# Kernel optimization log

Hardware: AMD Instinct MI355X
Metric: run time of the kernel (lower is better)

Reference implementation:

```python
import jax, jax.numpy as jnp
import numpy as np

# Model config (matches init_kwargs)
B, S = 4, 1024          # batch of equal-length prefill sequences (cu_seqlens = arange(B+1)*S)
H, KVH, D = 16, 4, 64   # query heads, kv heads (GQA), head_dim
SCALE = 0.125           # 1/sqrt(head_dim)
NUM_SLOTS = 8192        # paged-KV-cache total slots


def setup_inputs() -> dict:
    key = jax.random.key(0)
    k1, k2, k3 = jax.random.split(key, 3)
    N = B * S
    q = jax.random.normal(k1, (N, H * D), dtype=jnp.float32)
    k = jax.random.normal(k2, (N, KVH * D), dtype=jnp.float32)
    v = jax.random.normal(k3, (N, KVH * D), dtype=jnp.float32)
    k_cache = jnp.zeros((NUM_SLOTS, KVH * D), dtype=jnp.float32)
    v_cache = jnp.zeros((NUM_SLOTS, KVH * D), dtype=jnp.float32)
    slot_mapping = jnp.arange(N, dtype=jnp.int32)  # valid slots, no -1 entries
    return {"q": q, "k": k, "v": v, "k_cache": k_cache, "v_cache": v_cache,
            "slot_mapping": slot_mapping}


def _varlen_causal_attn(q, k, v):
    # q: [N, H*D], k/v: [N, KVH*D]; equal-length varlen batch -> [B, S, ...]
    qh = q.reshape(B, S, H, D)
    kh = k.reshape(B, S, KVH, D)
    vh = v.reshape(B, S, KVH, D)
    rep = H // KVH  # GQA: repeat kv heads to match query heads
    kh = jnp.repeat(kh, rep, axis=2)
    vh = jnp.repeat(vh, rep, axis=2)
    scores = jnp.einsum('bqhd,bkhd->bhqk', qh, kh) * SCALE
    causal = jnp.tril(jnp.ones((S, S), dtype=bool))
    scores = jnp.where(causal, scores, jnp.finfo(scores.dtype).min)
    p = jax.nn.softmax(scores, axis=-1)
    o = jnp.einsum('bhqk,bkhd->bqhd', p, vh)
    return o.reshape(B * S, H * D)


def reference(q, k, v, k_cache, v_cache, slot_mapping):
    # store_kvcache: scatter new k/v rows into the paged caches (Triton kernel equivalent)
    k_cache = k_cache.at[slot_mapping].set(k)
    v_cache = v_cache.at[slot_mapping].set(v)
    # prefill path: flash_attn_varlen_func(q, k, v, causal=True) on the fresh k/v
    o = _varlen_causal_attn(q, k, v)
    return o, k_cache, v_cache
```

## Files before the change

kernel.cpp:

```cpp
#include <hip/hip_runtime.h>
#include <hip/hip_bf16.h>

#define B_     4
#define S_     1024
#define H_     16
#define KVH_   4
#define D_     64
#define N_     (B_*S_)
#define SLOTS_ 8192
#define KVD_   (KVH_*D_)
#define HD_    (H_*D_)
#define SCL    (0.125f * 1.44269504f)

typedef __attribute__((ext_vector_type(8))) short bf16x8;
typedef __attribute__((ext_vector_type(4))) short bf16x4;
typedef __attribute__((ext_vector_type(4))) float f32x4;

__device__ __forceinline__ short4 f4tob4(float4 f){
    union { __hip_bfloat162 h[2]; short4 s; } u;
    u.h[0] = __float22bfloat162_rn(make_float2(f.x, f.y));
    u.h[1] = __float22bfloat162_rn(make_float2(f.z, f.w));
    return u.s;
}
__device__ __forceinline__ int swz(int row, int col){
    return row*64 + (col ^ ((row & 7) << 3));
}

__global__ __launch_bounds__(256) void copy_caches(
    const float4* __restrict__ kcin, const float4* __restrict__ vcin,
    float4* __restrict__ kc, float4* __restrict__ vc){
    int i = blockIdx.x*256 + threadIdx.x;
    kc[i] = kcin[i];
    vc[i] = vcin[i];
}

__global__ __launch_bounds__(256) void prep_kernel(
    const float* __restrict__ k, const float* __restrict__ v,
    const int* __restrict__ slot_map,
    float* __restrict__ kc, float* __restrict__ vc,
    short* __restrict__ Kb, short* __restrict__ Vtb)
{
    __shared__ short sv[64*68];
    const int tid = threadIdx.x;
    const int g   = blockIdx.x >> 4;
    const int s0  = (blockIdx.x & 15) * 64;
    const int b   = g >> 2, kvh = g & 3;

    const int sl = tid >> 2;
    const int cq = (tid & 3) * 16;

    const int n   = b*S_ + s0 + sl;
    const int pos = s0 + sl;
    const float4* kp = (const float4*)(k + (size_t)n*KVD_ + kvh*D_ + cq);
    const float4* vp = (const float4*)(v + (size_t)n*KVD_ + kvh*D_ + cq);
    const int s = slot_map[n];

    float4 kk[4], vv[4];
    #pragma unroll
    for (int j = 0; j < 4; ++j){ kk[j] = kp[j]; vv[j] = vp[j]; }

    if (s >= 0){
        float4* kcp = (float4*)(kc + (size_t)s*KVD_ + kvh*D_ + cq);
        float4* vcp = (float4*)(vc + (size_t)s*KVD_ + kvh*D_ + cq);
        #pragma unroll
        for (int j = 0; j < 4; ++j){ kcp[j] = kk[j]; vcp[j] = vv[j]; }
    }

    short* kbp = Kb + ((size_t)g*S_ + pos)*64 + cq;
    #pragma unroll
    for (int j = 0; j < 4; ++j)
        *(short4*)(kbp + j*4) = f4tob4(kk[j]);

    #pragma unroll
    for (int j = 0; j < 4; ++j)
        *(short4*)(&sv[sl*68 + cq + j*4]) = f4tob4(vv[j]);
    __syncthreads();

    const int d  = tid >> 2;
    const int sg = (tid & 3) * 16;
    union { short s[16]; bf16x8 v8[2]; } out;
    #pragma unroll
    for (int i = 0; i < 16; ++i)
        out.s[i] = sv[(sg + i)*68 + d];
    short* vtp = Vtb + ((size_t)g*64 + d)*S_ + s0 + sg;
    *(bf16x8*)(vtp)     = out.v8[0];
    *(bf16x8*)(vtp + 8) = out.v8[1];
}

__global__ __launch_bounds__(256, 2) void attn_kernel(
    const float* __restrict__ q, const short* __restrict__ Kb,
    const short* __restrict__ Vtb, float* __restrict__ o)
{
    __shared__ __align__(16) short sK[2][64*64];
    __shared__ __align__(16) short sV[2][64*64];

    const int tid  = threadIdx.x;
    const int wave = tid >> 6;
    const int lane = tid & 63;
    const int quad = lane >> 4;
    const int l16  = lane & 15;

    const int bid = blockIdx.x;
    const int g   = bid & 15;
    const int p   = bid >> 4;
    const int qtA = p, qtB = 63 - p;
    const int ntA = (qtA >> 2) + 1;
    const int ntB = (qtB >> 2) + 1;

    const int b = g >> 2, kvh = g & 3;
    const int h = kvh*4 + wave;

    bf16x8 qfA[2], qfB[2];
    {
        const float* qpA = q + ((size_t)(b*S_ + qtA*16 + l16))*HD_ + h*D_ + quad*8;
        const float* qpB = q + ((size_t)(b*S_ + qtB*16 + l16))*HD_ + h*D_ + quad*8;
        #pragma unroll
        for (int ks = 0; ks < 2; ++ks){
            float4 a0 = *(const float4*)(qpA + ks*32);
            float4 a1 = *(const float4*)(qpA + ks*32 + 4);
            float4 b0 = *(const float4*)(qpB + ks*32);
            float4 b1 = *(const float4*)(qpB + ks*32 + 4);
            a0.x*=SCL; a0.y*=SCL; a0.z*=SCL; a0.w*=SCL;
            a1.x*=SCL; a1.y*=SCL; a1.z*=SCL; a1.w*=SCL;
            b0.x*=SCL; b0.y*=SCL; b0.z*=SCL; b0.w*=SCL;
            b1.x*=SCL; b1.y*=SCL; b1.z*=SCL; b1.w*=SCL;
            union { short4 s[2]; bf16x8 v8; } ua, ub;
            ua.s[0] = f4tob4(a0); ua.s[1] = f4tob4(a1);
            ub.s[0] = f4tob4(b0); ub.s[1] = f4tob4(b1);
            qfA[ks] = ua.v8; qfB[ks] = ub.v8;
        }
    }

    f32x4 ofA[4], ofB[4];
    #pragma unroll
    for (int f2 = 0; f2 < 4; ++f2){
        ofA[f2] = (f32x4){0.f,0.f,0.f,0.f};
        ofB[f2] = (f32x4){0.f,0.f,0.f,0.f};
    }
    float lsA = 0.f, lsB = 0.f;
    const int qrowA = qtA*16 + l16, qrowB = qtB*16 + l16;

    const short* Kg = Kb  + (size_t)g*S_*64;
    const short* Vg = Vtb + (size_t)g*64*S_;

    const int rs = tid >> 2;
    const int cg = (tid & 3) * 16;

    bf16x8 kst[2], vst[2];
    kst[0] = *(const bf16x8*)(Kg + (size_t)rs*64 + cg);
    kst[1] = *(const bf16x8*)(Kg + (size_t)rs*64 + cg + 8);
    vst[0] = *(const bf16x8*)(Vg + (size_t)rs*S_ + cg);
    vst[1] = *(const bf16x8*)(Vg + (size_t)rs*S_ + cg + 8);

    auto pv_body = [&](const f32x4* sc, f32x4* of, float& lsum,
                       int qrow, bool diag, int t, const short* V_){
        bf16x4 pfrag[4];
        #pragma unroll
        for (int f = 0; f < 4; ++f){
            float4 pf;
            #pragma unroll
            for (int r = 0; r < 4; ++r){
                float pe = __builtin_amdgcn_exp2f(sc[f][r]);
                if (diag && (t*64 + f*16 + quad*4 + r > qrow)) pe = 0.f;
                lsum += pe;
                ((float*)&pf)[r] = pe;
            }
            union { short4 s; bf16x4 bv; } u; u.s = f4tob4(pf);
            pfrag[f] = u.bv;
        }
        #pragma unroll
        for (int f = 0; f < 4; ++f){
            #pragma unroll
            for (int f2 = 0; f2 < 4; ++f2){
                bf16x4 vf = *(const bf16x4*)(&V_[swz(f2*16 + l16, f*16 + quad*4)]);
                of[f2] = __builtin_amdgcn_mfma_f32_16x16x16bf16_1k(pfrag[f], vf, of[f2], 0, 0, 0);
            }
        }
    };

    for (int t = 0; t < ntB; ++t){
        short* K_ = (short*)sK[t & 1];
        short* V_ = (short*)sV[t & 1];
        *(bf16x8*)(&K_[swz(rs, cg)])     = kst[0];
        *(bf16x8*)(&K_[swz(rs, cg + 8)]) = kst[1];
        *(bf16x8*)(&V_[swz(rs, cg)])     = vst[0];
        *(bf16x8*)(&V_[swz(rs, cg + 8)]) = vst[1];
        if (t + 1 < ntB){
            kst[0] = *(const bf16x8*)(Kg + (size_t)((t+1)*64 + rs)*64 + cg);
            kst[1] = *(const bf16x8*)(Kg + (size_t)((t+1)*64 + rs)*64 + cg + 8);
            vst[0] = *(const bf16x8*)(Vg + (size_t)rs*S_ + (t+1)*64 + cg);
            vst[1] = *(const bf16x8*)(Vg + (size_t)rs*S_ + (t+1)*64 + cg + 8);
        }
        __syncthreads();

        bf16x8 kf[2][4];
        #pragma unroll
        for (int ks = 0; ks < 2; ++ks)
            #pragma unroll
            for (int f = 0; f < 4; ++f)
                kf[ks][f] = *(const bf16x8*)(&K_[swz(f*16 + l16, ks*32 + quad*8)]);

        const bool actA = (t < ntA);

        f32x4 scB[4];
        #pragma unroll
        for (int f = 0; f < 4; ++f) scB[f] = (f32x4){0.f,0.f,0.f,0.f};
        #pragma unroll
        for (int ks = 0; ks < 2; ++ks)
            #pragma unroll
            for (int f = 0; f < 4; ++f)
                scB[f] = __builtin_amdgcn_mfma_f32_16x16x32_bf16(kf[ks][f], qfB[ks], scB[f], 0, 0, 0);
        pv_body(scB, ofB, lsB, qrowB, t == ntB - 1, t, V_);

        if (actA){
            f32x4 scA[4];
            #pragma unroll
            for (int f = 0; f < 4; ++f) scA[f] = (f32x4){0.f,0.f,0.f,0.f};
            #pragma unroll
            for (int ks = 0; ks < 2; ++ks)
                #pragma unroll
                for (int f = 0; f < 4; ++f)
                    scA[f] = __builtin_amdgcn_mfma_f32_16x16x32_bf16(kf[ks][f], qfA[ks], scA[f], 0, 0, 0);
            pv_body(scA, ofA, lsA, qrowA, t == ntA - 1, t, V_);
        }
    }

    auto epilogue = [&](f32x4* of, float lsum, int qt){
        lsum += __shfl_xor(lsum, 16);
        lsum += __shfl_xor(lsum, 32);
        float linv[4];
        #pragma unroll
        for (int r = 0; r < 4; ++r)
            linv[r] = 1.f / __shfl(lsum, quad*4 + r);
        #pragma unroll
        for (int f2 = 0; f2 < 4; ++f2){
            #pragma unroll
            for (int r = 0; r < 4; ++r){
                const int row = qt*16 + quad*4 + r;
                o[((size_t)(b*S_ + row))*HD_ + h*D_ + f2*16 + l16] = of[f2][r] * linv[r];
            }
        }
    };
    epilogue(ofA, lsA, qtA);
    epilogue(ofB, lsB, qtB);
}

extern "C" void kernel_launch(void* const* d_in, const int* in_sizes, int n_in,
                              void* d_out, int out_size, void* d_ws, size_t ws_size,
                              hipStream_t stream){
    (void)in_sizes; (void)n_in; (void)out_size; (void)ws_size;
    const float* q     = (const float*)d_in[0];
    const float* k     = (const float*)d_in[1];
    const float* v     = (const float*)d_in[2];
    const float* kc_in = (const float*)d_in[3];
    const float* vc_in = (const float*)d_in[4];
    const int*   slot  = (const int*)d_in[5];

    float* o  = (float*)d_out;
    float* kc = o + (size_t)N_*HD_;
    float* vc = kc + (size_t)SLOTS_*KVD_;

    short* Kb = (short*)d_ws;
    short* Vt = Kb + (size_t)16*S_*64;

    copy_caches<<<(SLOTS_*64)/256, 256, 0, stream>>>(
        (const float4*)kc_in, (const float4*)vc_in, (float4*)kc, (float4*)vc);

    prep_kernel<<<256, 256, 0, stream>>>(k, v, slot, kc, vc, Kb, Vt);

    attn_kernel<<<512, 256, 0, stream>>>(q, Kb, Vt, o);
}
```

Measured before the change: 116.7 us.

## Fuse cache scatter into attention launch via inverse slot map, split heads per block

Replaces the standalone cache copy and the scatter inside prep with an inverse slot map, built by extra prep blocks. Extra blocks appended to the attention launch then write each cache row once, from either the new k/v or the old cache. This removes the copy-then-overwrite double write and lets the cache traffic overlap attention compute. Attention blocks shrink to 128 threads covering two heads, doubling the block count. The QK and PV phases for the two query tiles are interleaved to share V fragment loads. It adds an init kernel, and the split means K/V tiles are loaded into LDS twice per group.

```diff
diff --git a/kernel.cpp b/kernel.cpp
--- a/kernel.cpp
+++ b/kernel.cpp
@@ -12,6 +12,9 @@
 #define HD_    (H_*D_)
 #define SCL    (0.125f * 1.44269504f)
 
+#define NATT   1024
+#define NCACHE 4096
+
 typedef __attribute__((ext_vector_type(8))) short bf16x8;
 typedef __attribute__((ext_vector_type(4))) short bf16x4;
 typedef __attribute__((ext_vector_type(4))) float f32x4;
@@ -26,22 +29,23 @@
     return row*64 + (col ^ ((row & 7) << 3));
 }
 
-__global__ __launch_bounds__(256) void copy_caches(
-    const float4* __restrict__ kcin, const float4* __restrict__ vcin,
-    float4* __restrict__ kc, float4* __restrict__ vc){
-    int i = blockIdx.x*256 + threadIdx.x;
-    kc[i] = kcin[i];
-    vc[i] = vcin[i];
+__global__ void inv_init(int* __restrict__ inv){
+    inv[blockIdx.x*256 + threadIdx.x] = -1;
 }
 
 __global__ __launch_bounds__(256) void prep_kernel(
     const float* __restrict__ k, const float* __restrict__ v,
-    const int* __restrict__ slot_map,
-    float* __restrict__ kc, float* __restrict__ vc,
+    const int* __restrict__ slot_map, int* __restrict__ inv,
     short* __restrict__ Kb, short* __restrict__ Vtb)
 {
+    const int tid = threadIdx.x;
+    if (blockIdx.x >= 256){
+        int i = (blockIdx.x - 256)*256 + tid;
+        int s = slot_map[i];
+        if (s >= 0 && s < SLOTS_) inv[s] = i;
+        return;
+    }
     __shared__ short sv[64*68];
-    const int tid = threadIdx.x;
     const int g   = blockIdx.x >> 4;
     const int s0  = (blockIdx.x & 15) * 64;
     const int b   = g >> 2, kvh = g & 3;
@@ -50,23 +54,14 @@
     const int cq = (tid & 3) * 16;
 
     const int n   = b*S_ + s0 + sl;
-    const int pos = s0 + sl;
     const float4* kp = (const float4*)(k + (size_t)n*KVD_ + kvh*D_ + cq);
     const float4* vp = (const float4*)(v + (size_t)n*KVD_ + kvh*D_ + cq);
-    const int s = slot_map[n];
 
     float4 kk[4], vv[4];
     #pragma unroll
     for (int j = 0; j < 4; ++j){ kk[j] = kp[j]; vv[j] = vp[j]; }
 
-    if (s >= 0){
-        float4* kcp = (float4*)(kc + (size_t)s*KVD_ + kvh*D_ + cq);
-        float4* vcp = (float4*)(vc + (size_t)s*KVD_ + kvh*D_ + cq);
-        #pragma unroll
-        for (int j = 0; j < 4; ++j){ kcp[j] = kk[j]; vcp[j] = vv[j]; }
-    }
-
-    short* kbp = Kb + ((size_t)g*S_ + pos)*64 + cq;
+    short* kbp = Kb + ((size_t)g*S_ + s0 + sl)*64 + cq;
     #pragma unroll
     for (int j = 0; j < 4; ++j)
         *(short4*)(kbp + j*4) = f4tob4(kk[j]);
@@ -87,28 +82,49 @@
     *(bf16x8*)(vtp + 8) = out.v8[1];
 }
 
-__global__ __launch_bounds__(256, 2) void attn_kernel(
+__global__ __launch_bounds__(128, 2) void fused_kernel(
     const float* __restrict__ q, const short* __restrict__ Kb,
-    const short* __restrict__ Vtb, float* __restrict__ o)
+    const short* __restrict__ Vtb, float* __restrict__ o,
+    const float4* __restrict__ kin, const float4* __restrict__ vin,
+    const float4* __restrict__ kcin, const float4* __restrict__ vcin,
+    const int* __restrict__ inv,
+    float4* __restrict__ kc, float4* __restrict__ vc)
 {
+    const int tid = threadIdx.x;
+    const int bid = blockIdx.x;
+
+    if (bid >= NATT){
+        int i = (bid - NATT)*128 + tid;
+        int row = i >> 6;
+        int n = inv[row];
+        if (n >= 0){
+            int c = i & 63;
+            kc[i] = kin[(size_t)n*64 + c];
+            vc[i] = vin[(size_t)n*64 + c];
+        } else {
+            kc[i] = kcin[i];
+            vc[i] = vcin[i];
+        }
+        return;
+    }
+
     __shared__ __align__(16) short sK[2][64*64];
     __shared__ __align__(16) short sV[2][64*64];
 
-    const int tid  = threadIdx.x;
     const int wave = tid >> 6;
     const int lane = tid & 63;
     const int quad = lane >> 4;
     const int l16  = lane & 15;
 
-    const int bid = blockIdx.x;
-    const int g   = bid & 15;
-    const int p   = bid >> 4;
+    const int hp = bid & 1;
+    const int g  = (bid >> 1) & 15;
+    const int p  = bid >> 5;
     const int qtA = p, qtB = 63 - p;
     const int ntA = (qtA >> 2) + 1;
     const int ntB = (qtB >> 2) + 1;
 
     const int b = g >> 2, kvh = g & 3;
-    const int h = kvh*4 + wave;
+    const int h = kvh*4 + hp*2 + wave;
 
     bf16x8 qfA[2], qfB[2];
     {
@@ -143,55 +159,34 @@
     const short* Kg = Kb  + (size_t)g*S_*64;
     const short* Vg = Vtb + (size_t)g*64*S_;
 
-    const int rs = tid >> 2;
-    const int cg = (tid & 3) * 16;
-
-    bf16x8 kst[2], vst[2];
-    kst[0] = *(const bf16x8*)(Kg + (size_t)rs*64 + cg);
-    kst[1] = *(const bf16x8*)(Kg + (size_t)rs*64 + cg + 8);
-    vst[0] = *(const bf16x8*)(Vg + (size_t)rs*S_ + cg);
-    vst[1] = *(const bf16x8*)(Vg + (size_t)rs*S_ + cg + 8);
-
-    auto pv_body = [&](const f32x4* sc, f32x4* of, float& lsum,
-                       int qrow, bool diag, int t, const short* V_){
-        bf16x4 pfrag[4];
-        #pragma unroll
-        for (int f = 0; f < 4; ++f){
-            float4 pf;
-            #pragma unroll
-            for (int r = 0; r < 4; ++r){
-                float pe = __builtin_amdgcn_exp2f(sc[f][r]);
-                if (diag && (t*64 + f*16 + quad*4 + r > qrow)) pe = 0.f;
-                lsum += pe;
-                ((float*)&pf)[r] = pe;
-            }
-            union { short4 s; bf16x4 bv; } u; u.s = f4tob4(pf);
-            pfrag[f] = u.bv;
-        }
-        #pragma unroll
-        for (int f = 0; f < 4; ++f){
-            #pragma unroll
-            for (int f2 = 0; f2 < 4; ++f2){
-                bf16x4 vf = *(const bf16x4*)(&V_[swz(f2*16 + l16, f*16 + quad*4)]);
-                of[f2] = __builtin_amdgcn_mfma_f32_16x16x16bf16_1k(pfrag[f], vf, of[f2], 0, 0, 0);
-            }
-        }
-    };
+    const int rs = tid >> 1;
+    const int ch = (tid & 1) * 32;
+
+    bf16x8 kst[4], vst[4];
+    #pragma unroll
+    for (int j = 0; j < 4; ++j){
+        kst[j] = *(const bf16x8*)(Kg + (size_t)rs*64 + ch + j*8);
+        vst[j] = *(const bf16x8*)(Vg + (size_t)rs*S_ + ch + j*8);
+    }
 
     for (int t = 0; t < ntB; ++t){
         short* K_ = (short*)sK[t & 1];
         short* V_ = (short*)sV[t & 1];
-        *(bf16x8*)(&K_[swz(rs, cg)])     = kst[0];
-        *(bf16x8*)(&K_[swz(rs, cg + 8)]) = kst[1];
-        *(bf16x8*)(&V_[swz(rs, cg)])     = vst[0];
-        *(bf16x8*)(&V_[swz(rs, cg + 8)]) = vst[1];
+        #pragma unroll
+        for (int j = 0; j < 4; ++j){
+            *(bf16x8*)(&K_[swz(rs, ch + j*8)]) = kst[j];
+            *(bf16x8*)(&V_[swz(rs, ch + j*8)]) = vst[j];
+        }
         if (t + 1 < ntB){
-            kst[0] = *(const bf16x8*)(Kg + (size_t)((t+1)*64 + rs)*64 + cg);
-            kst[1] = *(const bf16x8*)(Kg + (size_t)((t+1)*64 + rs)*64 + cg + 8);
-            vst[0] = *(const bf16x8*)(Vg + (size_t)rs*S_ + (t+1)*64 + cg);
-            vst[1] = *(const bf16x8*)(Vg + (size_t)rs*S_ + (t+1)*64 + cg + 8);
+            #pragma unroll
+            for (int j = 0; j < 4; ++j){
+                kst[j] = *(const bf16x8*)(Kg + (size_t)((t+1)*64 + rs)*64 + ch + j*8);
+                vst[j] = *(const bf16x8*)(Vg + (size_t)rs*S_ + (t+1)*64 + ch + j*8);
+            }
         }
         __syncthreads();
+
+        const bool actA = (t < ntA);
 
         bf16x8 kf[2][4];
         #pragma unroll
@@ -200,28 +195,64 @@
             for (int f = 0; f < 4; ++f)
                 kf[ks][f] = *(const bf16x8*)(&K_[swz(f*16 + l16, ks*32 + quad*8)]);
 
-        const bool actA = (t < ntA);
-
-        f32x4 scB[4];
-        #pragma unroll
-        for (int f = 0; f < 4; ++f) scB[f] = (f32x4){0.f,0.f,0.f,0.f};
+        f32x4 scB[4], scA[4];
+        #pragma unroll
+        for (int f = 0; f < 4; ++f){
+            scB[f] = (f32x4){0.f,0.f,0.f,0.f};
+            scA[f] = (f32x4){0.f,0.f,0.f,0.f};
+        }
         #pragma unroll
         for (int ks = 0; ks < 2; ++ks)
             #pragma unroll
             for (int f = 0; f < 4; ++f)
                 scB[f] = __builtin_amdgcn_mfma_f32_16x16x32_bf16(kf[ks][f], qfB[ks], scB[f], 0, 0, 0);
-        pv_body(scB, ofB, lsB, qrowB, t == ntB - 1, t, V_);
-
         if (actA){
-            f32x4 scA[4];
-            #pragma unroll
-            for (int f = 0; f < 4; ++f) scA[f] = (f32x4){0.f,0.f,0.f,0.f};
             #pragma unroll
             for (int ks = 0; ks < 2; ++ks)
                 #pragma unroll
                 for (int f = 0; f < 4; ++f)
                     scA[f] = __builtin_amdgcn_mfma_f32_16x16x32_bf16(kf[ks][f], qfA[ks], scA[f], 0, 0, 0);
-            pv_body(scA, ofA, lsA, qrowA, t == ntA - 1, t, V_);
+        }
+
+        bf16x4 pfB[4], pfA[4];
+        #pragma unroll
+        for (int f = 0; f < 4; ++f){
+            float4 pf;
+            #pragma unroll
+            for (int r = 0; r < 4; ++r){
+                float pe = __builtin_amdgcn_exp2f(scB[f][r]);
+                if (t == ntB - 1 && (t*64 + f*16 + quad*4 + r > qrowB)) pe = 0.f;
+                lsB += pe;
+                ((float*)&pf)[r] = pe;
+            }
+            union { short4 s; bf16x4 bv; } u; u.s = f4tob4(pf);
+            pfB[f] = u.bv;
+        }
+        if (actA){
+            #pragma unroll
+            for (int f = 0; f < 4; ++f){
+                float4 pf;
+                #pragma unroll
+                for (int r = 0; r < 4; ++r){
+                    float pe = __builtin_amdgcn_exp2f(scA[f][r]);
+                    if (t == ntA - 1 && (t*64 + f*16 + quad*4 + r > qrowA)) pe = 0.f;
+                    lsA += pe;
+                    ((float*)&pf)[r] = pe;
+                }
+                union { short4 s; bf16x4 bv; } u; u.s = f4tob4(pf);
+                pfA[f] = u.bv;
+            }
+        }
+
+        #pragma unroll
+        for (int f = 0; f < 4; ++f){
+            #pragma unroll
+            for (int f2 = 0; f2 < 4; ++f2){
+                bf16x4 vf = *(const bf16x4*)(&V_[swz(f2*16 + l16, f*16 + quad*4)]);
+                ofB[f2] = __builtin_amdgcn_mfma_f32_16x16x16bf16_1k(pfB[f], vf, ofB[f2], 0, 0, 0);
+                if (actA)
+                    ofA[f2] = __builtin_amdgcn_mfma_f32_16x16x16bf16_1k(pfA[f], vf, ofA[f2], 0, 0, 0);
+            }
         }
     }
 
@@ -260,13 +291,17 @@
     float* kc = o + (size_t)N_*HD_;
     float* vc = kc + (size_t)SLOTS_*KVD_;
 
-    short* Kb = (short*)d_ws;
-    short* Vt = Kb + (size_t)16*S_*64;
-
-    copy_caches<<<(SLOTS_*64)/256, 256, 0, stream>>>(
-        (const float4*)kc_in, (const float4*)vc_in, (float4*)kc, (float4*)vc);
-
-    prep_kernel<<<256, 256, 0, stream>>>(k, v, slot, kc, vc, Kb, Vt);
-
-    attn_kernel<<<512, 256, 0, stream>>>(q, Kb, Vt, o);
-}
+    short* Kb  = (short*)d_ws;
+    short* Vt  = Kb + (size_t)16*S_*64;
+    int*   inv = (int*)((char*)d_ws + (4u << 20));
+
+    inv_init<<<SLOTS_/256, 256, 0, stream>>>(inv);
+
+    prep_kernel<<<256 + N_/256, 256, 0, stream>>>(k, v, slot, inv, Kb, Vt);
+
+    fused_kernel<<<NATT + NCACHE, 128, 0, stream>>>(
+        q, Kb, Vt, o,
+        (const float4*)k, (const float4*)v,
+        (const float4*)kc_in, (const float4*)vc_in, inv,
+        (float4*)kc, (float4*)vc);
+}
```

Result: slower. 123.4 us (+5.7%).
